# Optimization experiments

Measured on AMD Instinct MI355X. Metric: run time of the kernel, lower is better.

Reference implementation:

```python
import jax, jax.numpy as jnp
import numpy as np

DT = 0.5
DX = 0.01
MU_UP = 4e-05
PAD = 3  # 7x7 kernel // 2

_LAP = np.array([[0, 0, 0, 2, 0, 0, 0],
                 [0, 0, 0, -27, 0, 0, 0],
                 [0, 0, 0, 270, 0, 0, 0],
                 [2, -27, 270, -980, 270, -27, 2],
                 [0, 0, 0, 270, 0, 0, 0],
                 [0, 0, 0, -27, 0, 0, 0],
                 [0, 0, 0, 2, 0, 0, 0]], dtype=np.float32)
LAP_W = jnp.asarray(_LAP / (DX * DX) / 180.0)[None, None]  # [1,1,7,7]


def _laplace(x):
    # x: [B,1,H,W]; circular padding then valid conv (matches padding_mode='circular')
    xp = jnp.pad(x, ((0, 0), (0, 0), (PAD, PAD), (PAD, PAD)), mode='wrap')
    return jax.lax.conv_general_dilated(xp, LAP_W, (1, 1), 'VALID',
                                        dimension_numbers=('NCHW', 'OIHW', 'NCHW'))


def setup_inputs() -> dict:
    key = jax.random.key(0)
    ks = jax.random.split(key, 7)
    h = jax.random.uniform(ks[0], (16, 2, 1024, 1024), dtype=jnp.float32)
    CA = jax.random.uniform(ks[1], (), dtype=jnp.float32) - 0.5  # ~ -rand()+0.5
    CB = jax.random.uniform(ks[2], (), dtype=jnp.float32) - 0.5
    NA = -jax.random.uniform(ks[3], (), dtype=jnp.float32)
    NB = jax.random.uniform(ks[4], (), dtype=jnp.float32)
    f = 0.1 * jax.random.uniform(ks[5], (), dtype=jnp.float32)
    k = 0.1 * jax.random.uniform(ks[6], (), dtype=jnp.float32)
    return {"h": h, "CA": CA, "CB": CB, "NA": NA, "NB": NB, "f": f, "k": k}


def reference(h, CA, CB, NA, NB, f, k):
    mu_u = MU_UP * jax.nn.sigmoid(CA)
    mu_v = MU_UP * jax.nn.sigmoid(CB)

    def f_rhs(u, v):
        uv2 = u * v * v
        f_u = mu_u * _laplace(u) + NA * uv2 + f * (1.0 - u)
        f_v = mu_v * _laplace(v) + NB * uv2 - (k + f) * v
        return f_u, f_v

    u0 = h[:, 0:1]
    v0 = h[:, 1:2]
    k1_u, k1_v = f_rhs(u0, v0)
    k2_u, k2_v = f_rhs(u0 + k1_u * (DT / 2.0), v0 + k1_v * (DT / 2.0))
    k3_u, k3_v = f_rhs(u0 + k2_u * (DT / 2.0), v0 + k2_v * (DT / 2.0))
    k4_u, k4_v = f_rhs(u0 + k3_u * DT, v0 + k3_v * DT)
    u_next = u0 + DT * (k1_u + 2.0 * k2_u + 2.0 * k3_u + k4_u) / 6.0
    v_next = v0 + DT * (k1_v + 2.0 * k2_v + 2.0 * k3_v + k4_v) / 6.0
    return jnp.concatenate((u_next, v_next), axis=1)
```

## Files before the change

kernel.cpp:

```cpp
#include <hip/hip_runtime.h>


typedef float f2 __attribute__((ext_vector_type(2)));
typedef float f4 __attribute__((ext_vector_type(4)));

#define HROWS 64
#define NT    512
#define STEPS (HROWS + 24)

#define W0 ((-980.0f / 1e-4f) / 180.0f)
#define W1 ((  270.0f / 1e-4f) / 180.0f)
#define W2 (( -27.0f / 1e-4f) / 180.0f)
#define W3 ((   2.0f / 1e-4f) / 180.0f)

__device__ __forceinline__ f2 sp(float s) { f2 r; r.x = s; r.y = s; return r; }
__device__ __forceinline__ f2 pfma(float s, f2 a, f2 c) {
    return __builtin_elementwise_fma(sp(s), a, c);
}
__device__ __forceinline__ f2 lo2(f4 a) { return __builtin_shufflevector(a, a, 0, 1); }
__device__ __forceinline__ f2 hi2(f4 a) { return __builtin_shufflevector(a, a, 2, 3); }
__device__ __forceinline__ f4 cat(f2 a, f2 b) { return __builtin_shufflevector(a, b, 0, 1, 2, 3); }

struct Hq  { f2 m2, m1, p1, p2; };
struct Hq4 { f4 m2, m1, p1, p2; };

__device__ __forceinline__ Hq4 rdq4(const f4* __restrict__ L,
                                    int xm2, int xm1, int xp1, int xp2) {
    Hq4 q;
    q.m2 = L[xm2]; q.m1 = L[xm1]; q.p1 = L[xp1]; q.p2 = L[xp2];
    return q;
}

__device__ __forceinline__ void evalp7(f2 w0, f2 w1, f2 w2, f2 w3, f2 w4,
                                       f2 w5, f2 w6, const Hq& q,
                                       f2& lap, f2& ctr)
{
    ctr = w3;
    f2 vp = pfma(W1, w2 + w4, pfma(W2, w1 + w5, sp(W3) * (w0 + w6)));
    f2 m1 = __builtin_shufflevector(q.m1, ctr, 1, 2);
    f2 p1 = __builtin_shufflevector(ctr, q.p1, 1, 2);
    f2 m3 = __builtin_shufflevector(q.m2, q.m1, 1, 2);
    f2 p3 = __builtin_shufflevector(q.p1, q.p2, 1, 2);
    f2 hp = pfma(W1, m1 + p1, pfma(W2, q.m1 + q.p1, sp(W3) * (m3 + p3)));
    lap = pfma(W0, ctr, hp + vp);
}

__global__ __launch_bounds__(NT, 1) void rcnn_rk4_march(
    const float* __restrict__ h,
    const float* __restrict__ pCA, const float* __restrict__ pCB,
    const float* __restrict__ pNA, const float* __restrict__ pNB,
    const float* __restrict__ pf,  const float* __restrict__ pk,
    float* __restrict__ out)
{
    __shared__ f4 S[4][2][NT];

    const int tid = threadIdx.x;
    const int Y0  = blockIdx.x * HROWS;
    const int b   = blockIdx.z;

    const float NA = pNA[0], NB = pNB[0];
    const float ff = pf[0];
    const float kpf = pk[0] + pf[0];
    const float mu_u = 4e-5f / (1.0f + expf(-pCA[0]));
    const float mu_v = 4e-5f / (1.0f + expf(-pCB[0]));

    const size_t baseU = (size_t)b * 2u * 1048576u;
    const size_t baseV = baseU + 1048576u;
    const float* hU = h + baseU + 2 * tid;
    const float* hV = h + baseV + 2 * tid;
    float* oU = out + baseU + 2 * tid;
    float* oV = out + baseV + 2 * tid;

    const int xm2 = (tid - 2) & 511;
    const int xm1 = (tid - 1) & 511;
    const int xp1 = (tid + 1) & 511;
    const int xp2 = (tid + 2) & 511;

    f2 Uu[8], Uv[8], Du[8], Dv[8];
    f2 Y1u[8], Y1v[8], Y2u[8], Y2v[8], Y3u[8], Y3v[8];
    f2 ACu[8], ACv[8];

    const f2 z = sp(0.0f);
    #pragma unroll
    for (int j = 0; j < 8; ++j) {
        Uu[j]=z; Uv[j]=z; Du[j]=z; Dv[j]=z;
        Y1u[j]=z; Y1v[j]=z; Y2u[j]=z; Y2v[j]=z; Y3u[j]=z; Y3v[j]=z;
        ACu[j]=z; ACv[j]=z;
    }

    f2 pAu, pAv, pBu, pBv;
    {
        int r0 = (Y0 - 12) & 1023;
        int r1 = (Y0 - 11) & 1023;
        pAu = *(const f2*)(hU + (size_t)r0 * 1024);
        pAv = *(const f2*)(hV + (size_t)r0 * 1024);
        pBu = *(const f2*)(hU + (size_t)r1 * 1024);
        pBv = *(const f2*)(hV + (size_t)r1 * 1024);
    }

#define STEP(c, G1, G2, G3, G4, tb_)                                          \
  {                                                                           \
    const int t_ = (tb_) + (c);                                               \
                             \
    Du[(c)&7] = Uu[((c)+3)&7]; Dv[(c)&7] = Uv[((c)+3)&7];                     \
                                             \
    Uu[(c)&7] = ((c)&1) ? pBu : pAu;                                          \
    Uv[(c)&7] = ((c)&1) ? pBv : pAv;                                          \
                           \
    S[0][(c)&1][tid] = cat(Uu[((c)+6)&7], Uv[((c)+6)&7]);                     \
                                             \
    {                                                                         \
      int yn = (Y0 - 10 + t_) & 1023;                                         \
      f2 au = *(const f2*)(hU + (size_t)yn * 1024);                           \
      f2 av = *(const f2*)(hV + (size_t)yn * 1024);                           \
      if ((c)&1) { pBu = au; pBv = av; } else { pAu = au; pAv = av; }         \
    }                                                                         \
    if (G1) {                                         \
      Hq4 q = rdq4(&S[0][((c)+1)&1][0], xm2, xm1, xp1, xp2);                  \
      Hq qu = { lo2(q.m2), lo2(q.m1), lo2(q.p1), lo2(q.p2) };                 \
      Hq qv = { hi2(q.m2), hi2(q.m1), hi2(q.p1), hi2(q.p2) };                 \
      f2 lU, cU, lV, cV;                                                      \
      evalp7(Uu[((c)+2)&7], Uu[((c)+3)&7], Uu[((c)+4)&7], Uu[((c)+5)&7],      \
             Uu[((c)+6)&7], Uu[((c)+7)&7], Uu[(c)&7], qu, lU, cU);            \
      evalp7(Uv[((c)+2)&7], Uv[((c)+3)&7], Uv[((c)+4)&7], Uv[((c)+5)&7],      \
             Uv[((c)+6)&7], Uv[((c)+7)&7], Uv[(c)&7], qv, lV, cV);            \
      f2 uv2 = cU * cV * cV;                                                  \
      f2 kU = pfma(mu_u, lU, pfma(NA, uv2, pfma(-ff, cU, sp(ff))));           \
      f2 kV = pfma(mu_v, lV, pfma(NB, uv2, sp(-kpf) * cV));                   \
      Y1u[(c)&7] = pfma(0.25f, kU, cU);                                       \
      Y1v[(c)&7] = pfma(0.25f, kV, cV);                                       \
      S[1][(c)&1][tid] = cat(Y1u[((c)+6)&7], Y1v[((c)+6)&7]);                 \
    }                                                                         \
    if (G2) {                          \
      Hq4 q = rdq4(&S[1][((c)+1)&1][0], xm2, xm1, xp1, xp2);                  \
      Hq qu = { lo2(q.m2), lo2(q.m1), lo2(q.p1), lo2(q.p2) };                 \
      Hq qv = { hi2(q.m2), hi2(q.m1), hi2(q.p1), hi2(q.p2) };                 \
      f2 lU, cU, lV, cV;                                                      \
      evalp7(Y1u[((c)+2)&7], Y1u[((c)+3)&7], Y1u[((c)+4)&7], Y1u[((c)+5)&7],  \
             Y1u[((c)+6)&7], Y1u[((c)+7)&7], Y1u[(c)&7], qu, lU, cU);         \
      evalp7(Y1v[((c)+2)&7], Y1v[((c)+3)&7], Y1v[((c)+4)&7], Y1v[((c)+5)&7],  \
             Y1v[((c)+6)&7], Y1v[((c)+7)&7], Y1v[(c)&7], qv, lV, cV);         \
      f2 uv2 = cU * cV * cV;                                                  \
      f2 kU = pfma(mu_u, lU, pfma(NA, uv2, pfma(-ff, cU, sp(ff))));           \
      f2 kV = pfma(mu_v, lV, pfma(NB, uv2, sp(-kpf) * cV));                   \
      f2 bu = Du[((c)+7)&7], bv = Dv[((c)+7)&7];                \
      f2 nu = pfma(0.25f, kU, bu), nv = pfma(0.25f, kV, bv);                  \
      Y2u[(c)&7] = nu; Y2v[(c)&7] = nv;                                       \
      f2 aU = pfma(4.0f, Y1u[((c)+5)&7], sp(8.0f) * nu);                      \
      f2 aV = pfma(4.0f, Y1v[((c)+5)&7], sp(8.0f) * nv);                      \
      ACu[(c)&7] = pfma(-4.0f, bu, aU);                                       \
      ACv[(c)&7] = pfma(-4.0f, bv, aV);                                       \
      S[2][(c)&1][tid] = cat(Y2u[((c)+6)&7], Y2v[((c)+6)&7]);                 \
    }                                                                         \
    if (G3) {                                         \
      Hq4 q = rdq4(&S[2][((c)+1)&1][0], xm2, xm1, xp1, xp2);                  \
      Hq qu = { lo2(q.m2), lo2(q.m1), lo2(q.p1), lo2(q.p2) };                 \
      Hq qv = { hi2(q.m2), hi2(q.m1), hi2(q.p1), hi2(q.p2) };                 \
      f2 lU, cU, lV, cV;                                                      \
      evalp7(Y2u[((c)+2)&7], Y2u[((c)+3)&7], Y2u[((c)+4)&7], Y2u[((c)+5)&7],  \
             Y2u[((c)+6)&7], Y2u[((c)+7)&7], Y2u[(c)&7], qu, lU, cU);         \
      evalp7(Y2v[((c)+2)&7], Y2v[((c)+3)&7], Y2v[((c)+4)&7], Y2v[((c)+5)&7],  \
             Y2v[((c)+6)&7], Y2v[((c)+7)&7], Y2v[(c)&7], qv, lV, cV);         \
      f2 uv2 = cU * cV * cV;                                                  \
      f2 kU = pfma(mu_u, lU, pfma(NA, uv2, pfma(-ff, cU, sp(ff))));           \
      f2 kV = pfma(mu_v, lV, pfma(NB, uv2, sp(-kpf) * cV));                   \
      Y3u[(c)&7] = pfma(0.5f, kU, Du[((c)+4)&7]);               \
      Y3v[(c)&7] = pfma(0.5f, kV, Dv[((c)+4)&7]);                             \
      S[3][(c)&1][tid] = cat(Y3u[((c)+6)&7], Y3v[((c)+6)&7]);                 \
    }                                                                         \
    if (G4) {                         \
      Hq4 q = rdq4(&S[3][((c)+1)&1][0], xm2, xm1, xp1, xp2);                  \
      Hq qu = { lo2(q.m2), lo2(q.m1), lo2(q.p1), lo2(q.p2) };                 \
      Hq qv = { hi2(q.m2), hi2(q.m1), hi2(q.p1), hi2(q.p2) };                 \
      f2 lU, cU4, lV, cV4;                                                    \
      evalp7(Y3u[((c)+2)&7], Y3u[((c)+3)&7], Y3u[((c)+4)&7], Y3u[((c)+5)&7],  \
             Y3u[((c)+6)&7], Y3u[((c)+7)&7], Y3u[(c)&7], qu, lU, cU4);        \
      evalp7(Y3v[((c)+2)&7], Y3v[((c)+3)&7], Y3v[((c)+4)&7], Y3v[((c)+5)&7],  \
             Y3v[((c)+6)&7], Y3v[((c)+7)&7], Y3v[(c)&7], qv, lV, cV4);        \
      f2 uv2 = cU4 * cV4 * cV4;                                               \
      f2 kU = pfma(mu_u, lU, pfma(NA, uv2, pfma(-ff, cU4, sp(ff))));          \
      f2 kV = pfma(mu_v, lV, pfma(NB, uv2, sp(-kpf) * cV4));                  \
      f2 sU = pfma(4.0f, cU4, kU) + ACu[((c)+2)&7];             \
      f2 sV = pfma(4.0f, cV4, kV) + ACv[((c)+2)&7];                           \
      f2 oUq = sp(1.0f / 12.0f) * sU;                                         \
      f2 oVq = sp(1.0f / 12.0f) * sV;                                         \
      int yS = Y0 + t_ - 24;                                                  \
      *(f2*)(oU + (size_t)yS * 1024) = oUq;                                   \
      *(f2*)(oV + (size_t)yS * 1024) = oVq;                                   \
    }                                                                         \
    asm volatile("s_waitcnt lgkmcnt(0)" ::: "memory");                        \
    __builtin_amdgcn_s_barrier();                                             \
  }

    STEP(0,0,0,0,0, 0) STEP(1,0,0,0,0, 0) STEP(2,0,0,0,0, 0) STEP(3,0,0,0,0, 0)
    STEP(4,0,0,0,0, 0) STEP(5,0,0,0,0, 0) STEP(6,1,0,0,0, 0) STEP(7,1,0,0,0, 0)

    STEP(0,1,0,0,0, 8) STEP(1,1,0,0,0, 8) STEP(2,1,0,0,0, 8) STEP(3,1,0,0,0, 8)
    STEP(4,1,1,0,0, 8) STEP(5,1,1,0,0, 8) STEP(6,1,1,0,0, 8) STEP(7,1,1,0,0, 8)

    STEP(0,1,1,0,0,16) STEP(1,1,1,0,0,16) STEP(2,1,1,1,0,16) STEP(3,1,1,1,0,16)
    STEP(4,1,1,1,0,16) STEP(5,1,1,1,0,16) STEP(6,1,1,1,0,16) STEP(7,1,1,1,0,16)

    #pragma unroll 1
    for (int tb = 24; tb < STEPS; tb += 8) {
        STEP(0,1,1,1,1,tb) STEP(1,1,1,1,1,tb) STEP(2,1,1,1,1,tb) STEP(3,1,1,1,1,tb)
        STEP(4,1,1,1,1,tb) STEP(5,1,1,1,1,tb) STEP(6,1,1,1,1,tb) STEP(7,1,1,1,1,tb)
    }
#undef STEP
}

extern "C" void kernel_launch(void* const* d_in, const int* in_sizes, int n_in,
                              void* d_out, int out_size, void* d_ws, size_t ws_size,
                              hipStream_t stream) {
    const float* h   = (const float*)d_in[0];
    const float* pCA = (const float*)d_in[1];
    const float* pCB = (const float*)d_in[2];
    const float* pNA = (const float*)d_in[3];
    const float* pNB = (const float*)d_in[4];
    const float* pf  = (const float*)d_in[5];
    const float* pk  = (const float*)d_in[6];
    float* outp = (float*)d_out;

    dim3 grid(1024 / HROWS, 1, 16);
    dim3 block(NT);
    rcnn_rk4_march<<<grid, block, 0, stream>>>(h, pCA, pCB, pNA, pNB, pf, pk, outp);
}
```

Measured before the change: 93.04 us.

## Give each thread four columns, halve block size and rows per block

```diff
diff --git a/kernel.cpp b/kernel.cpp
--- a/kernel.cpp
+++ b/kernel.cpp
@@ -1,11 +1,10 @@
 #include <hip/hip_runtime.h>
 
 
-typedef float f2 __attribute__((ext_vector_type(2)));
 typedef float f4 __attribute__((ext_vector_type(4)));
 
-#define HROWS 64
-#define NT    512
+#define HROWS 32
+#define NT    256
 #define STEPS (HROWS + 24)
 
 #define W0 ((-980.0f / 1e-4f) / 180.0f)
@@ -13,46 +12,35 @@
 #define W2 (( -27.0f / 1e-4f) / 180.0f)
 #define W3 ((   2.0f / 1e-4f) / 180.0f)
 
-__device__ __forceinline__ f2 sp(float s) { f2 r; r.x = s; r.y = s; return r; }
-__device__ __forceinline__ f2 pfma(float s, f2 a, f2 c) {
-    return __builtin_elementwise_fma(sp(s), a, c);
-}
-__device__ __forceinline__ f2 lo2(f4 a) { return __builtin_shufflevector(a, a, 0, 1); }
-__device__ __forceinline__ f2 hi2(f4 a) { return __builtin_shufflevector(a, a, 2, 3); }
-__device__ __forceinline__ f4 cat(f2 a, f2 b) { return __builtin_shufflevector(a, b, 0, 1, 2, 3); }
-
-struct Hq  { f2 m2, m1, p1, p2; };
-struct Hq4 { f4 m2, m1, p1, p2; };
-
-__device__ __forceinline__ Hq4 rdq4(const f4* __restrict__ L,
-                                    int xm2, int xm1, int xp1, int xp2) {
-    Hq4 q;
-    q.m2 = L[xm2]; q.m1 = L[xm1]; q.p1 = L[xp1]; q.p2 = L[xp2];
-    return q;
-}
-
-__device__ __forceinline__ void evalp7(f2 w0, f2 w1, f2 w2, f2 w3, f2 w4,
-                                       f2 w5, f2 w6, const Hq& q,
-                                       f2& lap, f2& ctr)
+__device__ __forceinline__ f4 sp4(float s) { f4 r; r.x=s; r.y=s; r.z=s; r.w=s; return r; }
+__device__ __forceinline__ f4 pfma(float s, f4 a, f4 c) {
+    return __builtin_elementwise_fma(sp4(s), a, c);
+}
+
+__device__ __forceinline__ void evalp4(f4 w0, f4 w1, f4 w2, f4 w3, f4 w4,
+                                       f4 w5, f4 w6, f4 m, f4 p,
+                                       f4& lap, f4& ctr)
 {
     ctr = w3;
-    f2 vp = pfma(W1, w2 + w4, pfma(W2, w1 + w5, sp(W3) * (w0 + w6)));
-    f2 m1 = __builtin_shufflevector(q.m1, ctr, 1, 2);
-    f2 p1 = __builtin_shufflevector(ctr, q.p1, 1, 2);
-    f2 m3 = __builtin_shufflevector(q.m2, q.m1, 1, 2);
-    f2 p3 = __builtin_shufflevector(q.p1, q.p2, 1, 2);
-    f2 hp = pfma(W1, m1 + p1, pfma(W2, q.m1 + q.p1, sp(W3) * (m3 + p3)));
+    f4 vp = pfma(W1, w2 + w4, pfma(W2, w1 + w5, sp4(W3) * (w0 + w6)));
+    f4 sm1 = __builtin_shufflevector(m, ctr, 3, 4, 5, 6);
+    f4 sp1 = __builtin_shufflevector(ctr, p, 1, 2, 3, 4);
+    f4 sm2 = __builtin_shufflevector(m, ctr, 2, 3, 4, 5);
+    f4 sp2 = __builtin_shufflevector(ctr, p, 2, 3, 4, 5);
+    f4 sm3 = __builtin_shufflevector(m, ctr, 1, 2, 3, 4);
+    f4 sp3 = __builtin_shufflevector(ctr, p, 3, 4, 5, 6);
+    f4 hp = pfma(W1, sm1 + sp1, pfma(W2, sm2 + sp2, sp4(W3) * (sm3 + sp3)));
     lap = pfma(W0, ctr, hp + vp);
 }
 
-__global__ __launch_bounds__(NT, 1) void rcnn_rk4_march(
+__global__ __launch_bounds__(NT, 2) void rcnn_rk4_march(
     const float* __restrict__ h,
     const float* __restrict__ pCA, const float* __restrict__ pCB,
     const float* __restrict__ pNA, const float* __restrict__ pNB,
     const float* __restrict__ pf,  const float* __restrict__ pk,
     float* __restrict__ out)
 {
-    __shared__ f4 S[4][2][NT];
+    __shared__ f4 S[4][2][2][NT];
 
     const int tid = threadIdx.x;
     const int Y0  = blockIdx.x * HROWS;
@@ -66,21 +54,19 @@
 
     const size_t baseU = (size_t)b * 2u * 1048576u;
     const size_t baseV = baseU + 1048576u;
-    const float* hU = h + baseU + 2 * tid;
-    const float* hV = h + baseV + 2 * tid;
-    float* oU = out + baseU + 2 * tid;
-    float* oV = out + baseV + 2 * tid;
-
-    const int xm2 = (tid - 2) & 511;
-    const int xm1 = (tid - 1) & 511;
-    const int xp1 = (tid + 1) & 511;
-    const int xp2 = (tid + 2) & 511;
-
-    f2 Uu[8], Uv[8], Du[8], Dv[8];
-    f2 Y1u[8], Y1v[8], Y2u[8], Y2v[8], Y3u[8], Y3v[8];
-    f2 ACu[8], ACv[8];
-
-    const f2 z = sp(0.0f);
+    const float* hU = h + baseU + 4 * tid;
+    const float* hV = h + baseV + 4 * tid;
+    float* oU = out + baseU + 4 * tid;
+    float* oV = out + baseV + 4 * tid;
+
+    const int xm1 = (tid - 1) & 255;
+    const int xp1 = (tid + 1) & 255;
+
+    f4 Uu[8], Uv[8], Du[8], Dv[8];
+    f4 Y1u[8], Y1v[8], Y2u[8], Y2v[8], Y3u[8], Y3v[8];
+    f4 ACu[8], ACv[8];
+
+    const f4 z = sp4(0.0f);
     #pragma unroll
     for (int j = 0; j < 8; ++j) {
         Uu[j]=z; Uv[j]=z; Du[j]=z; Dv[j]=z;
@@ -88,14 +74,14 @@
         ACu[j]=z; ACv[j]=z;
     }
 
-    f2 pAu, pAv, pBu, pBv;
+    f4 pAu, pAv, pBu, pBv;
     {
         int r0 = (Y0 - 12) & 1023;
         int r1 = (Y0 - 11) & 1023;
-        pAu = *(const f2*)(hU + (size_t)r0 * 1024);
-        pAv = *(const f2*)(hV + (size_t)r0 * 1024);
-        pBu = *(const f2*)(hU + (size_t)r1 * 1024);
-        pBv = *(const f2*)(hV + (size_t)r1 * 1024);
+        pAu = *(const f4*)(hU + (size_t)r0 * 1024);
+        pAv = *(const f4*)(hV + (size_t)r0 * 1024);
+        pBu = *(const f4*)(hU + (size_t)r1 * 1024);
+        pBv = *(const f4*)(hV + (size_t)r1 * 1024);
     }
 
 #define STEP(c, G1, G2, G3, G4, tb_)                                          \
@@ -106,87 +92,87 @@
                                              \
     Uu[(c)&7] = ((c)&1) ? pBu : pAu;                                          \
     Uv[(c)&7] = ((c)&1) ? pBv : pAv;                                          \
-                           \
-    S[0][(c)&1][tid] = cat(Uu[((c)+6)&7], Uv[((c)+6)&7]);                     \
+                          \
+    S[0][(c)&1][0][tid] = Uu[((c)+6)&7];                                      \
+    S[0][(c)&1][1][tid] = Uv[((c)+6)&7];                                      \
                                              \
     {                                                                         \
       int yn = (Y0 - 10 + t_) & 1023;                                         \
-      f2 au = *(const f2*)(hU + (size_t)yn * 1024);                           \
-      f2 av = *(const f2*)(hV + (size_t)yn * 1024);                           \
+      f4 au = *(const f4*)(hU + (size_t)yn * 1024);                           \
+      f4 av = *(const f4*)(hV + (size_t)yn * 1024);                           \
       if ((c)&1) { pBu = au; pBv = av; } else { pAu = au; pAv = av; }         \
     }                                                                         \
     if (G1) {                                         \
-      Hq4 q = rdq4(&S[0][((c)+1)&1][0], xm2, xm1, xp1, xp2);                  \
-      Hq qu = { lo2(q.m2), lo2(q.m1), lo2(q.p1), lo2(q.p2) };                 \
-      Hq qv = { hi2(q.m2), hi2(q.m1), hi2(q.p1), hi2(q.p2) };                 \
-      f2 lU, cU, lV, cV;                                                      \
-      evalp7(Uu[((c)+2)&7], Uu[((c)+3)&7], Uu[((c)+4)&7], Uu[((c)+5)&7],      \
-             Uu[((c)+6)&7], Uu[((c)+7)&7], Uu[(c)&7], qu, lU, cU);            \
-      evalp7(Uv[((c)+2)&7], Uv[((c)+3)&7], Uv[((c)+4)&7], Uv[((c)+5)&7],      \
-             Uv[((c)+6)&7], Uv[((c)+7)&7], Uv[(c)&7], qv, lV, cV);            \
-      f2 uv2 = cU * cV * cV;                                                  \
-      f2 kU = pfma(mu_u, lU, pfma(NA, uv2, pfma(-ff, cU, sp(ff))));           \
-      f2 kV = pfma(mu_v, lV, pfma(NB, uv2, sp(-kpf) * cV));                   \
+      f4 mu = S[0][((c)+1)&1][0][xm1], pu = S[0][((c)+1)&1][0][xp1];          \
+      f4 mv = S[0][((c)+1)&1][1][xm1], pv = S[0][((c)+1)&1][1][xp1];          \
+      f4 lU, cU, lV, cV;                                                      \
+      evalp4(Uu[((c)+2)&7], Uu[((c)+3)&7], Uu[((c)+4)&7], Uu[((c)+5)&7],      \
+             Uu[((c)+6)&7], Uu[((c)+7)&7], Uu[(c)&7], mu, pu, lU, cU);        \
+      evalp4(Uv[((c)+2)&7], Uv[((c)+3)&7], Uv[((c)+4)&7], Uv[((c)+5)&7],      \
+             Uv[((c)+6)&7], Uv[((c)+7)&7], Uv[(c)&7], mv, pv, lV, cV);        \
+      f4 uv2 = cU * cV * cV;                                                  \
+      f4 kU = pfma(mu_u, lU, pfma(NA, uv2, pfma(-ff, cU, sp4(ff))));          \
+      f4 kV = pfma(mu_v, lV, pfma(NB, uv2, sp4(-kpf) * cV));                  \
       Y1u[(c)&7] = pfma(0.25f, kU, cU);                                       \
       Y1v[(c)&7] = pfma(0.25f, kV, cV);                                       \
-      S[1][(c)&1][tid] = cat(Y1u[((c)+6)&7], Y1v[((c)+6)&7]);                 \
-    }                                                                         \
-    if (G2) {                          \
-      Hq4 q = rdq4(&S[1][((c)+1)&1][0], xm2, xm1, xp1, xp2);                  \
-      Hq qu = { lo2(q.m2), lo2(q.m1), lo2(q.p1), lo2(q.p2) };                 \
-      Hq qv = { hi2(q.m2), hi2(q.m1), hi2(q.p1), hi2(q.p2) };                 \
-      f2 lU, cU, lV, cV;                                                      \
-      evalp7(Y1u[((c)+2)&7], Y1u[((c)+3)&7], Y1u[((c)+4)&7], Y1u[((c)+5)&7],  \
-             Y1u[((c)+6)&7], Y1u[((c)+7)&7], Y1u[(c)&7], qu, lU, cU);         \
-      evalp7(Y1v[((c)+2)&7], Y1v[((c)+3)&7], Y1v[((c)+4)&7], Y1v[((c)+5)&7],  \
-             Y1v[((c)+6)&7], Y1v[((c)+7)&7], Y1v[(c)&7], qv, lV, cV);         \
-      f2 uv2 = cU * cV * cV;                                                  \
-      f2 kU = pfma(mu_u, lU, pfma(NA, uv2, pfma(-ff, cU, sp(ff))));           \
-      f2 kV = pfma(mu_v, lV, pfma(NB, uv2, sp(-kpf) * cV));                   \
-      f2 bu = Du[((c)+7)&7], bv = Dv[((c)+7)&7];                \
-      f2 nu = pfma(0.25f, kU, bu), nv = pfma(0.25f, kV, bv);                  \
+      S[1][(c)&1][0][tid] = Y1u[((c)+6)&7];                                   \
+      S[1][(c)&1][1][tid] = Y1v[((c)+6)&7];                                   \
+    }                                                                         \
+    if (G2) {                               \
+      f4 mu = S[1][((c)+1)&1][0][xm1], pu = S[1][((c)+1)&1][0][xp1];          \
+      f4 mv = S[1][((c)+1)&1][1][xm1], pv = S[1][((c)+1)&1][1][xp1];          \
+      f4 lU, cU, lV, cV;                                                      \
+      evalp4(Y1u[((c)+2)&7], Y1u[((c)+3)&7], Y1u[((c)+4)&7], Y1u[((c)+5)&7],  \
+             Y1u[((c)+6)&7], Y1u[((c)+7)&7], Y1u[(c)&7], mu, pu, lU, cU);     \
+      evalp4(Y1v[((c)+2)&7], Y1v[((c)+3)&7], Y1v[((c)+4)&7], Y1v[((c)+5)&7],  \
+             Y1v[((c)+6)&7], Y1v[((c)+7)&7], Y1v[(c)&7], mv, pv, lV, cV);     \
+      f4 uv2 = cU * cV * cV;                                                  \
+      f4 kU = pfma(mu_u, lU, pfma(NA, uv2, pfma(-ff, cU, sp4(ff))));          \
+      f4 kV = pfma(mu_v, lV, pfma(NB, uv2, sp4(-kpf) * cV));                  \
+      f4 bu = Du[((c)+7)&7], bv = Dv[((c)+7)&7];                \
+      f4 nu = pfma(0.25f, kU, bu), nv = pfma(0.25f, kV, bv);                  \
       Y2u[(c)&7] = nu; Y2v[(c)&7] = nv;                                       \
-      f2 aU = pfma(4.0f, Y1u[((c)+5)&7], sp(8.0f) * nu);                      \
-      f2 aV = pfma(4.0f, Y1v[((c)+5)&7], sp(8.0f) * nv);                      \
+      f4 aU = pfma(4.0f, Y1u[((c)+5)&7], sp4(8.0f) * nu);                     \
+      f4 aV = pfma(4.0f, Y1v[((c)+5)&7], sp4(8.0f) * nv);                     \
       ACu[(c)&7] = pfma(-4.0f, bu, aU);                                       \
       ACv[(c)&7] = pfma(-4.0f, bv, aV);                                       \
-      S[2][(c)&1][tid] = cat(Y2u[((c)+6)&7], Y2v[((c)+6)&7]);                 \
+      S[2][(c)&1][0][tid] = Y2u[((c)+6)&7];                                   \
+      S[2][(c)&1][1][tid] = Y2v[((c)+6)&7];                                   \
     }                                                                         \
     if (G3) {                                         \
-      Hq4 q = rdq4(&S[2][((c)+1)&1][0], xm2, xm1, xp1, xp2);                  \
-      Hq qu = { lo2(q.m2), lo2(q.m1), lo2(q.p1), lo2(q.p2) };                 \
-      Hq qv = { hi2(q.m2), hi2(q.m1), hi2(q.p1), hi2(q.p2) };                 \
-      f2 lU, cU, lV, cV;                                                      \
-      evalp7(Y2u[((c)+2)&7], Y2u[((c)+3)&7], Y2u[((c)+4)&7], Y2u[((c)+5)&7],  \
-             Y2u[((c)+6)&7], Y2u[((c)+7)&7], Y2u[(c)&7], qu, lU, cU);         \
-      evalp7(Y2v[((c)+2)&7], Y2v[((c)+3)&7], Y2v[((c)+4)&7], Y2v[((c)+5)&7],  \
-             Y2v[((c)+6)&7], Y2v[((c)+7)&7], Y2v[(c)&7], qv, lV, cV);         \
-      f2 uv2 = cU * cV * cV;                                                  \
-      f2 kU = pfma(mu_u, lU, pfma(NA, uv2, pfma(-ff, cU, sp(ff))));           \
-      f2 kV = pfma(mu_v, lV, pfma(NB, uv2, sp(-kpf) * cV));                   \
+      f4 mu = S[2][((c)+1)&1][0][xm1], pu = S[2][((c)+1)&1][0][xp1];          \
+      f4 mv = S[2][((c)+1)&1][1][xm1], pv = S[2][((c)+1)&1][1][xp1];          \
+      f4 lU, cU, lV, cV;                                                      \
+      evalp4(Y2u[((c)+2)&7], Y2u[((c)+3)&7], Y2u[((c)+4)&7], Y2u[((c)+5)&7],  \
+             Y2u[((c)+6)&7], Y2u[((c)+7)&7], Y2u[(c)&7], mu, pu, lU, cU);     \
+      evalp4(Y2v[((c)+2)&7], Y2v[((c)+3)&7], Y2v[((c)+4)&7], Y2v[((c)+5)&7],  \
+             Y2v[((c)+6)&7], Y2v[((c)+7)&7], Y2v[(c)&7], mv, pv, lV, cV);     \
+      f4 uv2 = cU * cV * cV;                                                  \
+      f4 kU = pfma(mu_u, lU, pfma(NA, uv2, pfma(-ff, cU, sp4(ff))));          \
+      f4 kV = pfma(mu_v, lV, pfma(NB, uv2, sp4(-kpf) * cV));                  \
       Y3u[(c)&7] = pfma(0.5f, kU, Du[((c)+4)&7]);               \
       Y3v[(c)&7] = pfma(0.5f, kV, Dv[((c)+4)&7]);                             \
-      S[3][(c)&1][tid] = cat(Y3u[((c)+6)&7], Y3v[((c)+6)&7]);                 \
+      S[3][(c)&1][0][tid] = Y3u[((c)+6)&7];                                   \
+      S[3][(c)&1][1][tid] = Y3v[((c)+6)&7];                                   \
     }                                                                         \
     if (G4) {                         \
-      Hq4 q = rdq4(&S[3][((c)+1)&1][0], xm2, xm1, xp1, xp2);                  \
-      Hq qu = { lo2(q.m2), lo2(q.m1), lo2(q.p1), lo2(q.p2) };                 \
-      Hq qv = { hi2(q.m2), hi2(q.m1), hi2(q.p1), hi2(q.p2) };                 \
-      f2 lU, cU4, lV, cV4;                                                    \
-      evalp7(Y3u[((c)+2)&7], Y3u[((c)+3)&7], Y3u[((c)+4)&7], Y3u[((c)+5)&7],  \
-             Y3u[((c)+6)&7], Y3u[((c)+7)&7], Y3u[(c)&7], qu, lU, cU4);        \
-      evalp7(Y3v[((c)+2)&7], Y3v[((c)+3)&7], Y3v[((c)+4)&7], Y3v[((c)+5)&7],  \
-             Y3v[((c)+6)&7], Y3v[((c)+7)&7], Y3v[(c)&7], qv, lV, cV4);        \
-      f2 uv2 = cU4 * cV4 * cV4;                                               \
-      f2 kU = pfma(mu_u, lU, pfma(NA, uv2, pfma(-ff, cU4, sp(ff))));          \
-      f2 kV = pfma(mu_v, lV, pfma(NB, uv2, sp(-kpf) * cV4));                  \
-      f2 sU = pfma(4.0f, cU4, kU) + ACu[((c)+2)&7];             \
-      f2 sV = pfma(4.0f, cV4, kV) + ACv[((c)+2)&7];                           \
-      f2 oUq = sp(1.0f / 12.0f) * sU;                                         \
-      f2 oVq = sp(1.0f / 12.0f) * sV;                                         \
+      f4 mu = S[3][((c)+1)&1][0][xm1], pu = S[3][((c)+1)&1][0][xp1];          \
+      f4 mv = S[3][((c)+1)&1][1][xm1], pv = S[3][((c)+1)&1][1][xp1];          \
+      f4 lU, cU4, lV, cV4;                                                    \
+      evalp4(Y3u[((c)+2)&7], Y3u[((c)+3)&7], Y3u[((c)+4)&7], Y3u[((c)+5)&7],  \
+             Y3u[((c)+6)&7], Y3u[((c)+7)&7], Y3u[(c)&7], mu, pu, lU, cU4);    \
+      evalp4(Y3v[((c)+2)&7], Y3v[((c)+3)&7], Y3v[((c)+4)&7], Y3v[((c)+5)&7],  \
+             Y3v[((c)+6)&7], Y3v[((c)+7)&7], Y3v[(c)&7], mv, pv, lV, cV4);    \
+      f4 uv2 = cU4 * cV4 * cV4;                                               \
+      f4 kU = pfma(mu_u, lU, pfma(NA, uv2, pfma(-ff, cU4, sp4(ff))));         \
+      f4 kV = pfma(mu_v, lV, pfma(NB, uv2, sp4(-kpf) * cV4));                 \
+      f4 sU = pfma(4.0f, cU4, kU) + ACu[((c)+2)&7];             \
+      f4 sV = pfma(4.0f, cV4, kV) + ACv[((c)+2)&7];                           \
+      f4 oUq = sp4(1.0f / 12.0f) * sU;                                        \
+      f4 oVq = sp4(1.0f / 12.0f) * sV;                                        \
       int yS = Y0 + t_ - 24;                                                  \
-      *(f2*)(oU + (size_t)yS * 1024) = oUq;                                   \
-      *(f2*)(oV + (size_t)yS * 1024) = oVq;                                   \
+      *(f4*)(oU + (size_t)yS * 1024) = oUq;                                   \
+      *(f4*)(oV + (size_t)yS * 1024) = oVq;                                   \
     }                                                                         \
     asm volatile("s_waitcnt lgkmcnt(0)" ::: "memory");                        \
     __builtin_amdgcn_s_barrier();                                             \
```

Result: slower. 348.2 us (+274.2%).
